# Kernel tuning notes

Measured on AMD Instinct MI355X. Metric: run time of the kernel, lower is better.

Reference implementation:

```python
import jax, jax.numpy as jnp
import numpy as np


def setup_inputs() -> dict:
    key = jax.random.key(0)
    ks = jax.random.split(key, 12)
    B, N, Din, D, K = 2, 1024, 64, 64, 24
    s = lambda fan_in: 1.0 / np.sqrt(fan_in)
    return {
        "feature": jax.random.normal(ks[0], (B, N, Din), jnp.float32),
        "xyz": jax.random.normal(ks[1], (B, N, 3), jnp.float32),
        "pw1": jax.random.uniform(ks[2], (Din, D), jnp.float32, -s(Din), s(Din)),
        "pb1": jax.random.uniform(ks[3], (D,), jnp.float32, -s(Din), s(Din)),
        "pw2": jax.random.uniform(ks[4], (D, D), jnp.float32, -s(D), s(D)),
        "pb2": jax.random.uniform(ks[5], (D,), jnp.float32, -s(D), s(D)),
        "rw": jax.random.uniform(ks[6], (3, D * D), jnp.float32, -s(3), s(3)),
        "rb": jax.random.uniform(ks[7], (D * D,), jnp.float32, -s(3), s(3)),
        "sw": jax.random.uniform(ks[8], (D, D), jnp.float32, -s(D), s(D)),
        "sb": jax.random.uniform(ks[9], (D,), jnp.float32, -s(D), s(D)),
        "knn_num": 24,
    }


def reference(feature, xyz, pw1, pb1, pw2, pb2, rw, rb, sw, sb, knn_num):
    B, N, _ = feature.shape
    D = pw2.shape[1]
    K = knn_num
    # KNN over xyz (squared euclidean distances, smallest K)
    sq = jnp.sum(xyz * xyz, axis=-1)  # [B,N]
    d2 = sq[:, :, None] + sq[:, None, :] - 2.0 * jnp.einsum('bnc,bmc->bnm', xyz, xyz)
    _, idx = jax.lax.top_k(-d2, K)  # [B,N,K]
    bidx = jnp.arange(B)[:, None, None]
    rel = xyz[bidx, idx] - xyz[:, :, None, :]  # [B,N,K,3]
    # prefix MLP: relu(Linear -> ReLU -> Linear)
    feat = jax.nn.relu(jax.nn.relu(feature @ pw1 + pb1) @ pw2 + pb2)  # [B,N,D]
    # per-edge weight generation + softmax over (K*D)
    w = (rel @ rw + rb).reshape(B, N, K * D, D)
    w = jax.nn.softmax(w, axis=-2)
    # gather neighbor features and aggregate
    gv = feat[bidx, idx].reshape(B, N, K * D)  # [B,N,K*D]
    out = jnp.einsum('bnm,bnmd->bnd', gv, w)  # [B,N,D]
    out = out @ sw + sb
    return (out, N)
```

## Files before the change

kernel.cpp:

```cpp
#include <hip/hip_runtime.h>
#include <math.h>

#define BB 2
#define NN 1024
#define DD 64
#define KK 24
#define NPTS (BB * NN)

#if __has_builtin(__builtin_amdgcn_exp2f)
#define EXP2(x) __builtin_amdgcn_exp2f(x)
#else
#define EXP2(x) exp2f(x)
#endif

typedef float v2f __attribute__((ext_vector_type(2)));

static __device__ __forceinline__ v2f pk_fma(v2f a, v2f b, v2f c) {
    v2f d;
    asm("v_pk_fma_f32 %0, %1, %2, %3" : "=v"(d) : "v"(a), "v"(b), "v"(c));
    return d;
}
static __device__ __forceinline__ v2f pk_add(v2f a, v2f b) {
    v2f d;
    asm("v_pk_add_f32 %0, %1, %2" : "=v"(d) : "v"(a), "v"(b));
    return d;
}


__global__ __launch_bounds__(256) void prep_mlp_knn_kernel(
    const float* __restrict__ feature, const float* __restrict__ xyz,
    const float* __restrict__ pw1, const float* __restrict__ pb1,
    const float* __restrict__ pw2, const float* __restrict__ pb2,
    const float* __restrict__ rw, const float* __restrict__ rb,
    float* __restrict__ feat, int* __restrict__ idx_out,
    float4* __restrict__ rwP) {
    int bid = blockIdx.x;
    int tid = threadIdx.x;

    if (bid < 512) {
        int r = tid >> 6;
        int d = tid & 63;
        int row = bid * 4 + r;
        __shared__ float s_in[4][64];
        __shared__ float s_h[4][64];
        s_in[r][d] = feature[row * 64 + d];
        __syncthreads();
        float h = pb1[d];
#pragma unroll
        for (int i = 0; i < 64; i++) h = __builtin_fmaf(s_in[r][i], pw1[i * 64 + d], h);
        h = fmaxf(h, 0.f);
        s_h[r][d] = h;
        __syncthreads();
        float f = pb2[d];
#pragma unroll
        for (int i = 0; i < 64; i++) f = __builtin_fmaf(s_h[r][i], pw2[i * 64 + d], f);
        f = fmaxf(f, 0.f);
        feat[row * 64 + d] = f;
    } else if (bid < 528) {
        const float LOG2E = 1.4426950408889634f;
        int t = (bid - 512) * 256 + tid;
        float4 v;
        v.x = rw[t] * LOG2E;
        v.y = rw[4096 + t] * LOG2E;
        v.z = rw[8192 + t] * LOG2E;
        v.w = rb[t] * LOG2E;
        rwP[t] = v;
    } else {
        int w = tid >> 6;
        int lane = tid & 63;
        int pt = (bid - 528) * 4 + w;
        int b = pt >> 10;
        int n = pt & 1023;
        const float* xb = xyz + (size_t)b * NN * 3;
        float xn = xb[n * 3 + 0], yn = xb[n * 3 + 1], zn = xb[n * 3 + 2];
        float sqn = xn * xn + yn * yn + zn * zn;
        float dist[16];
#pragma unroll
        for (int c = 0; c < 16; c++) {
            int m = c * 64 + lane;
            float xm = xb[m * 3 + 0], ym = xb[m * 3 + 1], zm = xb[m * 3 + 2];
            float sqm = xm * xm + ym * ym + zm * zm;
            float dot = xn * xm + yn * ym + zn * zm;
            dist[c] = sqn + sqm - 2.0f * dot;
        }
        for (int r = 0; r < KK; r++) {
            float best = 3.4e38f;
            int bi = 1 << 30;
#pragma unroll
            for (int c = 0; c < 16; c++) {
                if (dist[c] < best) {
                    best = dist[c];
                    bi = c * 64 + lane;
                }
            }
#pragma unroll
            for (int off = 32; off >= 1; off >>= 1) {
                float ob = __shfl_down(best, off);
                int oi = __shfl_down(bi, off);
                if (ob < best || (ob == best && oi < bi)) {
                    best = ob;
                    bi = oi;
                }
            }
            bi = __shfl(bi, 0);
            if ((bi & 63) == lane) dist[bi >> 6] = 3.4e38f;
            if (lane == 0) idx_out[pt * KK + r] = bi;
        }
    }
}

#define GVS 28
__global__ __launch_bounds__(256, 1) void agg_kernel(const float* __restrict__ xyz,
                                                     const float* __restrict__ feat,
                                                     const int* __restrict__ idx,
                                                     const float4* __restrict__ rwP,
                                                     const float* __restrict__ sw,
                                                     const float* __restrict__ sb,
                                                     float* __restrict__ out) {
    int pt = blockIdx.x;
    int b = pt >> 10;
    int n = pt & 1023;
    int tid = threadIdx.x;
    int w = tid >> 6;
    int d = tid & 63;

    __shared__ __align__(8) float s_relT[3][28];
    __shared__ __align__(16) float s_gvt[64][GVS];
    __shared__ float s_red[8][64];
    __shared__ float s_pre[64];

    const float* xb = xyz + (size_t)b * NN * 3;
    if (tid < KK * 3) {
        int k = tid % KK, c = tid / KK;
        int nb = idx[pt * KK + k];
        s_relT[c][k] = xb[nb * 3 + c] - xb[n * 3 + c];
    }
    for (int t = tid; t < KK * 64; t += 256) {
        int k = t >> 6, j = t & 63;
        int nb = idx[pt * KK + k];
        s_gvt[j][k] = feat[((size_t)b * NN + nb) * 64 + j];
    }
    __syncthreads();

    v2f rx[12], ry[12], rz[12];
#pragma unroll
    for (int k = 0; k < 12; k++) {
        rx[k] = *(const v2f*)&s_relT[0][2 * k];
        ry[k] = *(const v2f*)&s_relT[1][2 * k];
        rz[k] = *(const v2f*)&s_relT[2][2 * k];
    }

    v2f l0 = {0.f, 0.f}, l1 = {0.f, 0.f}, a0 = {0.f, 0.f}, a1 = {0.f, 0.f};
    int col0 = (w * 16) * 64 + d;
    float4 rv = rwP[col0];
    for (int jj = 0; jj < 16; jj++) {
        int j = w * 16 + jj;
        float4 rvn = rv;
        if (jj < 15) rvn = rwP[col0 + (jj + 1) * 64];
        v2f R0 = {rv.x, rv.x}, R1 = {rv.y, rv.y}, R2 = {rv.z, rv.z}, RB = {rv.w, rv.w};
        const float4* g4 = (const float4*)(&s_gvt[j][0]);
#pragma unroll
        for (int q = 0; q < 6; q++) {
            float4 g = g4[q];
            v2f ga = {g.x, g.y};
            v2f gb = {g.z, g.w};
            v2f t0 = pk_fma(rx[2 * q], R0, pk_fma(ry[2 * q], R1, pk_fma(rz[2 * q], R2, RB)));
            v2f t1 = pk_fma(rx[2 * q + 1], R0, pk_fma(ry[2 * q + 1], R1, pk_fma(rz[2 * q + 1], R2, RB)));
            v2f e0 = {EXP2(t0.x), EXP2(t0.y)};
            v2f e1 = {EXP2(t1.x), EXP2(t1.y)};
            l0 = pk_add(l0, e0);
            l1 = pk_add(l1, e1);
            a0 = pk_fma(ga, e0, a0);
            a1 = pk_fma(gb, e1, a1);
        }
        rv = rvn;
    }
    s_red[w][d] = l0.x + l0.y + l1.x + l1.y;
    s_red[4 + w][d] = a0.x + a0.y + a1.x + a1.y;
    __syncthreads();
    if (tid < 64) {
        float L = s_red[0][d] + s_red[1][d] + s_red[2][d] + s_red[3][d];
        float A = s_red[4][d] + s_red[5][d] + s_red[6][d] + s_red[7][d];
        s_pre[d] = A / L;
    }
    __syncthreads();
    float part = 0.f;
#pragma unroll
    for (int dd = 0; dd < 16; dd++) {
        int drow = w * 16 + dd;
        part = __builtin_fmaf(s_pre[drow], sw[drow * 64 + d], part);
    }
    s_red[w][d] = part;
    __syncthreads();
    if (tid < 64) {
        float o = s_red[0][d] + s_red[1][d] + s_red[2][d] + s_red[3][d] + sb[d];
        out[(size_t)pt * 64 + d] = o;
    }
    if (pt == 0 && tid == 0) out[(size_t)NPTS * 64] = 1024.0f;
}

extern "C" void kernel_launch(void* const* d_in, const int* in_sizes, int n_in,
                              void* d_out, int out_size, void* d_ws, size_t ws_size,
                              hipStream_t stream) {
    const float* feature = (const float*)d_in[0];
    const float* xyz = (const float*)d_in[1];
    const float* pw1 = (const float*)d_in[2];
    const float* pb1 = (const float*)d_in[3];
    const float* pw2 = (const float*)d_in[4];
    const float* pb2 = (const float*)d_in[5];
    const float* rw = (const float*)d_in[6];
    const float* rb = (const float*)d_in[7];
    const float* sw = (const float*)d_in[8];
    const float* sb = (const float*)d_in[9];
    float* out = (float*)d_out;

    char* ws = (char*)d_ws;
    float* feat = (float*)(ws);
    int* idx = (int*)(ws + 524288);
    float4* rwP = (float4*)(ws + 720896);

    prep_mlp_knn_kernel<<<1040, 256, 0, stream>>>(feature, xyz, pw1, pb1, pw2, pb2,
                                                  rw, rb, feat, idx, rwP);
    agg_kernel<<<NPTS, 256, 0, stream>>>(xyz, feat, idx, rwP, sw, sb, out);
}
```

Baseline: 131.7 us.

## Split aggregation work across waves by neighbor instead of by feature column

Each wave now handles 6 of the 24 neighbors across all 64 j columns, rather than all 24 neighbors for 16 columns. The relative coordinates are computed per wave directly in registers, and gathered features are stored in a pair-interleaved shared layout so one float4 read serves two j values. rwP is streamed over all 64 columns with prefetch, which quadruples the per-wave global loads of rwP but cuts the register needs for rel. Launch bounds move to 4 blocks per CU to raise occupancy.

```diff
diff --git a/kernel.cpp b/kernel.cpp
--- a/kernel.cpp
+++ b/kernel.cpp
@@ -109,8 +109,7 @@
     }
 }
 
-#define GVS 28
-__global__ __launch_bounds__(256, 1) void agg_kernel(const float* __restrict__ xyz,
+__global__ __launch_bounds__(256, 4) void agg_kernel(const float* __restrict__ xyz,
                                                      const float* __restrict__ feat,
                                                      const int* __restrict__ idx,
                                                      const float4* __restrict__ rwP,
@@ -124,59 +123,84 @@
     int w = tid >> 6;
     int d = tid & 63;
 
-    __shared__ __align__(8) float s_relT[3][28];
-    __shared__ __align__(16) float s_gvt[64][GVS];
+    __shared__ __align__(16) float s_gvp[12][64][2];
     __shared__ float s_red[8][64];
     __shared__ float s_pre[64];
 
     const float* xb = xyz + (size_t)b * NN * 3;
-    if (tid < KK * 3) {
-        int k = tid % KK, c = tid / KK;
-        int nb = idx[pt * KK + k];
-        s_relT[c][k] = xb[nb * 3 + c] - xb[n * 3 + c];
-    }
+
     for (int t = tid; t < KK * 64; t += 256) {
         int k = t >> 6, j = t & 63;
         int nb = idx[pt * KK + k];
-        s_gvt[j][k] = feat[((size_t)b * NN + nb) * 64 + j];
-    }
-    __syncthreads();
-
-    v2f rx[12], ry[12], rz[12];
-#pragma unroll
-    for (int k = 0; k < 12; k++) {
-        rx[k] = *(const v2f*)&s_relT[0][2 * k];
-        ry[k] = *(const v2f*)&s_relT[1][2 * k];
-        rz[k] = *(const v2f*)&s_relT[2][2 * k];
-    }
-
-    v2f l0 = {0.f, 0.f}, l1 = {0.f, 0.f}, a0 = {0.f, 0.f}, a1 = {0.f, 0.f};
-    int col0 = (w * 16) * 64 + d;
-    float4 rv = rwP[col0];
-    for (int jj = 0; jj < 16; jj++) {
-        int j = w * 16 + jj;
-        float4 rvn = rv;
-        if (jj < 15) rvn = rwP[col0 + (jj + 1) * 64];
-        v2f R0 = {rv.x, rv.x}, R1 = {rv.y, rv.y}, R2 = {rv.z, rv.z}, RB = {rv.w, rv.w};
-        const float4* g4 = (const float4*)(&s_gvt[j][0]);
-#pragma unroll
-        for (int q = 0; q < 6; q++) {
-            float4 g = g4[q];
-            v2f ga = {g.x, g.y};
-            v2f gb = {g.z, g.w};
-            v2f t0 = pk_fma(rx[2 * q], R0, pk_fma(ry[2 * q], R1, pk_fma(rz[2 * q], R2, RB)));
-            v2f t1 = pk_fma(rx[2 * q + 1], R0, pk_fma(ry[2 * q + 1], R1, pk_fma(rz[2 * q + 1], R2, RB)));
+        s_gvp[k >> 1][j][k & 1] = feat[((size_t)b * NN + nb) * 64 + j];
+    }
+
+    float cx = xb[n * 3 + 0], cy = xb[n * 3 + 1], cz = xb[n * 3 + 2];
+    v2f rxp[3], ryp[3], rzp[3];
+#pragma unroll
+    for (int p = 0; p < 3; p++) {
+        int nb0 = idx[pt * KK + w * 6 + 2 * p];
+        int nb1 = idx[pt * KK + w * 6 + 2 * p + 1];
+        rxp[p] = (v2f){xb[nb0 * 3 + 0] - cx, xb[nb1 * 3 + 0] - cx};
+        ryp[p] = (v2f){xb[nb0 * 3 + 1] - cy, xb[nb1 * 3 + 1] - cy};
+        rzp[p] = (v2f){xb[nb0 * 3 + 2] - cz, xb[nb1 * 3 + 2] - cz};
+    }
+    __syncthreads();
+
+    v2f l0 = {0.f, 0.f}, l1 = {0.f, 0.f}, l2 = {0.f, 0.f};
+    v2f a0 = {0.f, 0.f}, a1 = {0.f, 0.f}, a2 = {0.f, 0.f};
+    int kp0 = 3 * w;
+
+    float4 G0 = *(const float4*)&s_gvp[kp0 + 0][0][0];
+    float4 G1 = *(const float4*)&s_gvp[kp0 + 1][0][0];
+    float4 G2 = *(const float4*)&s_gvp[kp0 + 2][0][0];
+    float4 rv0 = rwP[d];
+    float4 rv1 = rwP[64 + d];
+
+    for (int jg = 0; jg < 32; jg++) {
+        int jn = ((jg + 1) & 31) * 2;
+        float4 G0n = *(const float4*)&s_gvp[kp0 + 0][jn][0];
+        float4 G1n = *(const float4*)&s_gvp[kp0 + 1][jn][0];
+        float4 G2n = *(const float4*)&s_gvp[kp0 + 2][jn][0];
+        float4 rv0n = rwP[jn * 64 + d];
+        float4 rv1n = rwP[(jn + 1) * 64 + d];
+
+        {
+            v2f B0 = {rv0.x, rv0.x}, B1 = {rv0.y, rv0.y}, B2 = {rv0.z, rv0.z}, BBv = {rv0.w, rv0.w};
+            v2f t0 = pk_fma(rxp[0], B0, pk_fma(ryp[0], B1, pk_fma(rzp[0], B2, BBv)));
+            v2f t1 = pk_fma(rxp[1], B0, pk_fma(ryp[1], B1, pk_fma(rzp[1], B2, BBv)));
+            v2f t2 = pk_fma(rxp[2], B0, pk_fma(ryp[2], B1, pk_fma(rzp[2], B2, BBv)));
             v2f e0 = {EXP2(t0.x), EXP2(t0.y)};
             v2f e1 = {EXP2(t1.x), EXP2(t1.y)};
+            v2f e2 = {EXP2(t2.x), EXP2(t2.y)};
             l0 = pk_add(l0, e0);
             l1 = pk_add(l1, e1);
-            a0 = pk_fma(ga, e0, a0);
-            a1 = pk_fma(gb, e1, a1);
-        }
-        rv = rvn;
-    }
-    s_red[w][d] = l0.x + l0.y + l1.x + l1.y;
-    s_red[4 + w][d] = a0.x + a0.y + a1.x + a1.y;
+            l2 = pk_add(l2, e2);
+            a0 = pk_fma((v2f){G0.x, G0.y}, e0, a0);
+            a1 = pk_fma((v2f){G1.x, G1.y}, e1, a1);
+            a2 = pk_fma((v2f){G2.x, G2.y}, e2, a2);
+        }
+        {
+            v2f B0 = {rv1.x, rv1.x}, B1 = {rv1.y, rv1.y}, B2 = {rv1.z, rv1.z}, BBv = {rv1.w, rv1.w};
+            v2f t0 = pk_fma(rxp[0], B0, pk_fma(ryp[0], B1, pk_fma(rzp[0], B2, BBv)));
+            v2f t1 = pk_fma(rxp[1], B0, pk_fma(ryp[1], B1, pk_fma(rzp[1], B2, BBv)));
+            v2f t2 = pk_fma(rxp[2], B0, pk_fma(ryp[2], B1, pk_fma(rzp[2], B2, BBv)));
+            v2f e0 = {EXP2(t0.x), EXP2(t0.y)};
+            v2f e1 = {EXP2(t1.x), EXP2(t1.y)};
+            v2f e2 = {EXP2(t2.x), EXP2(t2.y)};
+            l0 = pk_add(l0, e0);
+            l1 = pk_add(l1, e1);
+            l2 = pk_add(l2, e2);
+            a0 = pk_fma((v2f){G0.z, G0.w}, e0, a0);
+            a1 = pk_fma((v2f){G1.z, G1.w}, e1, a1);
+            a2 = pk_fma((v2f){G2.z, G2.w}, e2, a2);
+        }
+        G0 = G0n; G1 = G1n; G2 = G2n;
+        rv0 = rv0n; rv1 = rv1n;
+    }
+
+    s_red[w][d] = (l0.x + l0.y) + (l1.x + l1.y) + (l2.x + l2.y);
+    s_red[4 + w][d] = (a0.x + a0.y) + (a1.x + a1.y) + (a2.x + a2.y);
     __syncthreads();
     if (tid < 64) {
         float L = s_red[0][d] + s_red[1][d] + s_red[2][d] + s_red[3][d];
```

New measurement: 137.9 us. +4.7%, slower.
